# Performance work log

Hardware: AMD Instinct MI355X
Metric: run time of the kernel (lower is better)

Reference implementation:

```python
import jax, jax.numpy as jnp
import numpy as np

B, N, D, EMB, H, W = 32, 20, 512, 512, 64, 64
TEMP = 10.0
EPS_IN = 1e-5


def setup_inputs() -> dict:
    key = jax.random.key(0)
    ks = jax.random.split(key, 12)
    fvisu = jax.random.normal(ks[0], (B, D, H, W), dtype=jnp.float32)
    fword = jax.random.normal(ks[1], (B, N, D), dtype=jnp.float32)
    context_score = jax.random.uniform(ks[2], (B, N), dtype=jnp.float32)
    # contiguous valid-token mask: lengths in [3, N-1] so CLS/SEP zeroing stays in range
    lengths = jax.random.randint(ks[3], (B,), 3, N)  # < N
    word_mask = (jnp.arange(N)[None, :] < lengths[:, None]).astype(jnp.int32)
    # params (kaiming-ish scale)
    def kinit(k, shape, fan_in):
        return jax.random.normal(k, shape, dtype=jnp.float32) * np.sqrt(2.0 / fan_in)
    attn_map_w = kinit(ks[4], (EMB // 2, D), D)          # Conv1d(512,256,1)
    attn_map_b = jnp.zeros((EMB // 2,), jnp.float32)
    attn_score_w = kinit(ks[5], (EMB // 2,), EMB // 2)   # Conv1d(256,1,1)
    attn_score_b = jnp.zeros((), jnp.float32)
    gamma_w = kinit(ks[6], (2 * EMB, D), D)              # Linear(512, 1024)
    gamma_b = jnp.zeros((2 * EMB,), jnp.float32)
    conv1_w = kinit(ks[7], (EMB, D), D)                  # Conv2d(512,512,1)
    conv1_b = jnp.zeros((EMB,), jnp.float32)
    return {
        "fvisu": fvisu, "fword": fword, "context_score": context_score,
        "attn_map_w": attn_map_w, "attn_map_b": attn_map_b,
        "attn_score_w": attn_score_w, "attn_score_b": attn_score_b,
        "gamma_w": gamma_w, "gamma_b": gamma_b,
        "conv1_w": conv1_w, "conv1_b": conv1_b,
        "word_mask": word_mask,
    }


def mask_softmax(attn_score, word_mask):
    # score = softmax(attn_score * T) over words
    score = jax.nn.softmax(attn_score * TEMP, axis=1)
    n = attn_score.shape[1]
    idx = jnp.arange(n)[None, :]
    m = word_mask[:, :n].astype(jnp.float32)
    m = m * (idx != 0)                                   # zero CLS
    s = m.sum(axis=1).astype(jnp.int32)                  # sum AFTER zeroing pos 0
    m = m * (idx != s[:, None])                          # zero SEP (last valid)
    ms = score * m
    return ms / (ms.sum(axis=1, keepdims=True) + 1e-8)


def reference(fvisu, fword, context_score, attn_map_w, attn_map_b,
              attn_score_w, attn_score_b, gamma_w, gamma_b,
              conv1_w, conv1_b, word_mask):
    # fword: [B,N,D] -> fw: [B,D,N]
    fw = jnp.transpose(fword, (0, 2, 1))
    # tile_visu: mean over spatial -> [B,D,1]
    tile_visu = jnp.mean(fvisu.reshape(fvisu.shape[0], fvisu.shape[1], -1), axis=2, keepdims=True)
    # prod fusion
    context_tile = tile_visu * fw * context_score[:, None, :]           # [B,D,N]
    attn_feat = jnp.tanh(jnp.einsum('oc,bcn->bon', attn_map_w, context_tile) + attn_map_b[None, :, None])
    attn_score = jnp.einsum('c,bcn->bn', attn_score_w, attn_feat) + attn_score_b  # [B,N]
    mask_score = mask_softmax(attn_score, word_mask)
    attn_lang_my = mask_score[:, None, :] * fw                          # [B,D,N]
    attn_lang = jnp.einsum('bn,bnd->bd', mask_score, fword)             # [B,D]
    # FiLM params
    film = attn_lang @ gamma_w.T + gamma_b                              # [B,2*EMB]
    gammas = jnp.tanh(film[:, :EMB])[:, :, None, None]
    betas = jnp.tanh(film[:, EMB:])[:, :, None, None]
    # conv1 (1x1) + InstanceNorm2d (no affine)
    fmodu = jnp.einsum('oc,bchw->bohw', conv1_w, fvisu) + conv1_b[None, :, None, None]
    mu = jnp.mean(fmodu, axis=(2, 3), keepdims=True)
    var = jnp.var(fmodu, axis=(2, 3), keepdims=True)
    fmodu = (fmodu - mu) * jax.lax.rsqrt(var + EPS_IN)
    fmodu = jax.nn.relu(gammas * fmodu + betas)
    return fmodu, attn_lang_my, attn_score
```

## Files before the change

kernel.cpp:

```cpp
#include <hip/hip_runtime.h>
#include <hip/hip_bf16.h>
#include <stdint.h>

#define NW 20
#define CD 512

typedef __attribute__((ext_vector_type(8))) short bhalf8;
typedef __attribute__((ext_vector_type(4))) float floatx4;

__device__ __forceinline__ uint16_t f2bf(float f){
    __hip_bfloat16 h = __float2bfloat16(f);
    return __builtin_bit_cast(uint16_t, h);
}
__device__ __forceinline__ float bf2f(uint16_t u){
    return __uint_as_float(((uint32_t)u) << 16);
}
__device__ __forceinline__ int hsw(int r){ return ((r >> 1) ^ (r >> 2)) & 7; }

__device__ __forceinline__ void gload16(const void* g, void* l){
    __builtin_amdgcn_global_load_lds(
        (const __attribute__((address_space(1))) uint32_t*)g,
        (__attribute__((address_space(3))) uint32_t*)l, 16, 0, 0);
}

__global__ void GroundTextBlock_context_49761491091856_kernel(int* p){ if (p) *p = 0; }

__global__ __launch_bounds__(256) void kprep(const float* __restrict__ w,
                                             uint16_t* __restrict__ warr){
    int ot = blockIdx.x >> 3, ks = blockIdx.x & 7;
    uint16_t* dst = warr + (size_t)blockIdx.x * 8192;
    for (int i = threadIdx.x; i < 8192; i += 256){
        int o = i >> 6, ke = i & 63;
        float v = w[(size_t)(ot * 128 + o) * 512 + ks * 64 + ke];
        int byteoff = o * 128 + ((((ke >> 3) ^ hsw(o)) << 4)) + ((ke & 7) << 1);
        dst[byteoff >> 1] = f2bf(v);
    }
}

__global__ __launch_bounds__(256) void kprepB(const float* __restrict__ fvisu,
                                              float* __restrict__ out0){
    __shared__ __align__(16) uint8_t Bb[16384];
    __shared__ float tsum[CD];

    int b = blockIdx.x >> 5, jt = blockIdx.x & 31;
    int t = threadIdx.x, lane = t & 63;
    int cs0 = t >> 5, js = t & 31;
    int j0 = jt * 128;

    for (int ks = 0; ks < 8; ++ks){
        if (ks) __syncthreads();
        int k0 = ks * 64;
        #pragma unroll
        for (int blk = 0; blk < 2; ++blk){
            int cs = cs0 + blk * 8;
            float va[4][4];
            #pragma unroll
            for (int ci = 0; ci < 4; ++ci){
                const float* src = fvisu + (((size_t)(b * CD + k0 + cs * 4 + ci)) << 12) + j0 + js * 4;
                float4 v = *(const float4*)src;
                va[ci][0] = v.x; va[ci][1] = v.y; va[ci][2] = v.z; va[ci][3] = v.w;
            }
            #pragma unroll
            for (int ci = 0; ci < 4; ++ci){
                float s = va[ci][0] + va[ci][1] + va[ci][2] + va[ci][3];
                s += __shfl_xor(s, 1);  s += __shfl_xor(s, 2);
                s += __shfl_xor(s, 4);  s += __shfl_xor(s, 8);
                s += __shfl_xor(s, 16);
                if ((lane & 31) == 0) tsum[k0 + cs * 4 + ci] = s;
            }
            int unit = cs >> 1, half = cs & 1;
            #pragma unroll
            for (int jj = 0; jj < 4; ++jj){
                int j = js * 4 + jj;
                uint2 p;
                p.x = (uint32_t)f2bf(va[0][jj]) | ((uint32_t)f2bf(va[1][jj]) << 16);
                p.y = (uint32_t)f2bf(va[2][jj]) | ((uint32_t)f2bf(va[3][jj]) << 16);
                *(uint2*)(Bb + j * 128 + ((unit ^ hsw(j)) << 4) + half * 8) = p;
            }
        }
        __syncthreads();
        #pragma unroll
        for (int it = 0; it < 4; ++it){
            int off = it * 4096 + t * 16;
            int rrow = jt * 16 + ks * 2 + (off >> 13);
            uint8_t* dst = (uint8_t*)out0 + (((size_t)(b * CD + rrow)) << 14) + 8192 + (off & 8191);
            *(float4*)dst = *(const float4*)(Bb + off);
        }
    }
    __syncthreads();
    float* tp = out0 + (((size_t)(b * CD + jt)) << 12);
    tp[t] = tsum[t];
    tp[t + 256] = tsum[t + 256];
}

__global__ __launch_bounds__(256) void kgemm(const uint16_t* __restrict__ warr,
                                             float* __restrict__ out0){
    __shared__ __align__(16) uint8_t Ab[16384];
    __shared__ __align__(16) uint8_t Bb[16384];

    int lid = (int)((blockIdx.x & 7) * 512 + (blockIdx.x >> 3));
    int ot = lid & 3, jt = (lid >> 2) & 31, b = lid >> 7;

    int t = threadIdx.x;
    int lane = t & 63, wv = t >> 6;
    int wr = wv >> 1, wc = wv & 1;
    int l15 = lane & 15, l4 = lane >> 4;
    int j0 = jt * 128;

    floatx4 acc[4][4];
    #pragma unroll
    for (int m = 0; m < 4; ++m)
        #pragma unroll
        for (int n = 0; n < 4; ++n)
            acc[m][n] = (floatx4){0.f, 0.f, 0.f, 0.f};

    for (int ks = 0; ks < 8; ++ks){
        if (ks) __syncthreads();
        {
            const uint8_t* asrc = (const uint8_t*)warr + (size_t)(ot * 8 + ks) * 16384;
            #pragma unroll
            for (int it = 0; it < 4; ++it){
                int lin = it * 4096 + t * 16;
                gload16(asrc + lin, Ab + lin);
            }
        }
        #pragma unroll
        for (int it = 0; it < 4; ++it){
            int off = it * 4096 + t * 16;
            int rrow = jt * 16 + ks * 2 + (off >> 13);
            const uint8_t* src = (const uint8_t*)out0 + (((size_t)(b * CD + rrow)) << 14) + 8192 + (off & 8191);
            gload16(src, Bb + off);
        }
        __syncthreads();
        #pragma unroll
        for (int ksl = 0; ksl < 2; ++ksl){
            bhalf8 af[4], bfr[4];
            #pragma unroll
            for (int m = 0; m < 4; ++m){
                int o = wr * 64 + m * 16 + l15;
                int u = (ksl * 4 + l4) ^ hsw(o);
                af[m] = *(const bhalf8*)(Ab + o * 128 + (u << 4));
            }
            #pragma unroll
            for (int n = 0; n < 4; ++n){
                int j = wc * 64 + n * 16 + l15;
                int u = (ksl * 4 + l4) ^ hsw(j);
                bfr[n] = *(const bhalf8*)(Bb + j * 128 + (u << 4));
            }
            #pragma unroll
            for (int m = 0; m < 4; ++m)
                #pragma unroll
                for (int n = 0; n < 4; ++n)
                    acc[m][n] = __builtin_amdgcn_mfma_f32_16x16x32_bf16(af[m], bfr[n], acc[m][n], 0, 0, 0);
        }
    }
    uint16_t* sbase = (uint16_t*)out0;
    #pragma unroll
    for (int m = 0; m < 4; ++m){
        #pragma unroll
        for (int r = 0; r < 4; ++r){
            int o = ot * 128 + wr * 64 + m * 16 + l4 * 4 + r;
            uint16_t* row = sbase + ((size_t)(b * CD + o) << 13);
            #pragma unroll
            for (int n = 0; n < 4; ++n)
                row[j0 + wc * 64 + n * 16 + l15] = f2bf(acc[m][n][r]);
        }
    }
}

__global__ __launch_bounds__(256) void kattn(
    const float* __restrict__ fword, const float* __restrict__ cscore,
    const float* __restrict__ amw, const float* __restrict__ amb,
    const float* __restrict__ asw, const float* __restrict__ asb,
    const float* __restrict__ gw, const float* __restrict__ gb,
    const int* __restrict__ wmask, const float* __restrict__ out0,
    float* __restrict__ out1, float* __restrict__ out2,
    float* __restrict__ gam_arr, float* __restrict__ bet_arr)
{
    int b = blockIdx.x, t = threadIdx.x;
    __shared__ __align__(16) float fws[NW][CD];
    __shared__ __align__(16) float tl[CD];
    __shared__ __align__(16) float al[CD];
    __shared__ float css[NW];
    __shared__ int wm[NW];
    __shared__ float wred[4][NW];
    __shared__ float sc[NW];
    __shared__ float ms[NW];

    #pragma unroll
    for (int dd = 0; dd < 2; ++dd){
        int c = t + dd * 256;
        float s = 0.f;
        #pragma unroll 8
        for (int j2 = 0; j2 < 32; ++j2)
            s += out0[(((size_t)(b * CD + j2)) << 12) + c];
        tl[c] = s * (1.f / 4096.f);
    }
    {
        const float4* src = (const float4*)(fword + (size_t)b * NW * CD);
        float4* dst = (float4*)&fws[0][0];
        for (int i = t; i < NW * CD / 4; i += 256) dst[i] = src[i];
    }
    if (t < NW){ css[t] = cscore[b * NW + t]; wm[t] = wmask[b * NW + t]; }
    __syncthreads();

    int o = t;
    float a[NW];
    #pragma unroll
    for (int n = 0; n < NW; ++n) a[n] = 0.f;
    {
        const float4* wrp = (const float4*)(amw + (size_t)o * CD);
        for (int c4 = 0; c4 < 128; ++c4){
            float4 wvv = wrp[c4];
            float4 tv = *(const float4*)(tl + c4 * 4);
            float wtx = wvv.x * tv.x, wty = wvv.y * tv.y, wtz = wvv.z * tv.z, wtw = wvv.w * tv.w;
            #pragma unroll
            for (int n = 0; n < NW; ++n){
                const float4 f = *(const float4*)(&fws[n][c4 * 4]);
                a[n] += wtx * f.x + wty * f.y + wtz * f.z + wtw * f.w;
            }
        }
    }
    {
        float aswo = asw[o], ambo = amb[o];
        #pragma unroll
        for (int n = 0; n < NW; ++n){
            float fo = aswo * tanhf(a[n] * css[n] + ambo);
            #pragma unroll
            for (int m = 1; m <= 32; m <<= 1) fo += __shfl_xor(fo, m);
            if ((t & 63) == 0) wred[t >> 6][n] = fo;
        }
    }
    __syncthreads();
    if (t < NW){
        float s = asb[0] + wred[0][t] + wred[1][t] + wred[2][t] + wred[3][t];
        sc[t] = s;
        out2[b * NW + t] = s;
    }
    __syncthreads();
    if (t < 64){
        float logit = (t < NW) ? sc[t] * 10.f : -1e30f;
        float mx = logit;
        #pragma unroll
        for (int m = 32; m >= 1; m >>= 1) mx = fmaxf(mx, __shfl_xor(mx, m));
        float e = (t < NW) ? expf(logit - mx) : 0.f;
        float den = e;
        #pragma unroll
        for (int m = 32; m >= 1; m >>= 1) den += __shfl_xor(den, m);
        float p = e / den;
        float m0 = (t > 0 && t < NW) ? (float)wm[t] : 0.f;
        float cnt = m0;
        #pragma unroll
        for (int m = 32; m >= 1; m >>= 1) cnt += __shfl_xor(cnt, m);
        int sidx = (int)(cnt + 0.5f);
        float m1 = (t == sidx) ? 0.f : m0;
        float msv = p * m1;
        float d2 = msv;
        #pragma unroll
        for (int m = 32; m >= 1; m >>= 1) d2 += __shfl_xor(d2, m);
        d2 += 1e-8f;
        if (t < NW) ms[t] = msv / d2;
    }
    __syncthreads();
    #pragma unroll
    for (int dd = 0; dd < 2; ++dd){
        int d = t + dd * 256;
        float acc_ = 0.f;
        float pk[NW];
        #pragma unroll
        for (int n = 0; n < NW; ++n){
            float v = ms[n] * fws[n][d];
            acc_ += v;
            pk[n] = v;
        }
        al[d] = acc_;
        float4* dst = (float4*)(out1 + (size_t)b * CD * NW + (size_t)d * NW);
        #pragma unroll
        for (int i = 0; i < NW / 4; ++i)
            dst[i] = make_float4(pk[i * 4], pk[i * 4 + 1], pk[i * 4 + 2], pk[i * 4 + 3]);
    }
    __syncthreads();
    #pragma unroll
    for (int kk = 0; kk < 4; ++kk){
        int k = kk * 256 + t;
        const float4* gr = (const float4*)(gw + (size_t)k * CD);
        float s = gb[k];
        for (int c4 = 0; c4 < 128; ++c4){
            float4 g4 = gr[c4];
            float4 a4 = *(const float4*)(al + c4 * 4);
            s += g4.x * a4.x + g4.y * a4.y + g4.z * a4.z + g4.w * a4.w;
        }
        float tv = tanhf(s);
        if (k < CD) gam_arr[b * CD + k] = tv;
        else        bet_arr[b * CD + (k - CD)] = tv;
    }
}

__global__ __launch_bounds__(256) void knormstat(
    float* __restrict__ out0, const float* __restrict__ gam_arr,
    const float* __restrict__ bet_arr)
{
    int bo = blockIdx.x, t = threadIdx.x;
    const uint16_t* srow = (const uint16_t*)out0 + ((size_t)bo << 13);
    float x[16];
    float s = 0.f, q = 0.f;
    #pragma unroll
    for (int h = 0; h < 2; ++h){
        uint4 v = *(const uint4*)(srow + (size_t)(h * 256 + t) * 8);
        uint32_t w[4] = {v.x, v.y, v.z, v.w};
        #pragma unroll
        for (int i = 0; i < 4; ++i){
            float x0 = bf2f((uint16_t)(w[i] & 0xffffu));
            float x1 = bf2f((uint16_t)(w[i] >> 16));
            x[h * 8 + i * 2]     = x0;
            x[h * 8 + i * 2 + 1] = x1;
            s += x0 + x1; q += x0 * x0 + x1 * x1;
        }
    }
    #pragma unroll
    for (int m = 1; m <= 32; m <<= 1){ s += __shfl_xor(s, m); q += __shfl_xor(q, m); }
    __shared__ float ss[4], qq[4];
    if ((t & 63) == 0){ ss[t >> 6] = s; qq[t >> 6] = q; }
    __syncthreads();
    float S = ss[0] + ss[1] + ss[2] + ss[3];
    float Q = qq[0] + qq[1] + qq[2] + qq[3];
    float mu = S * (1.f / 4096.f);
    float var = Q * (1.f / 4096.f) - mu * mu;
    float rs = rsqrtf(var + 1e-5f);
    float g = gam_arr[bo], be = bet_arr[bo];
    float4* drow = (float4*)(out0 + ((size_t)bo << 12));
    #pragma unroll
    for (int h = 0; h < 2; ++h){
        #pragma unroll
        for (int gix = 0; gix < 2; ++gix){
            float4 w4;
            w4.x = fmaxf(0.f, g * ((x[h * 8 + gix * 4 + 0] - mu) * rs) + be);
            w4.y = fmaxf(0.f, g * ((x[h * 8 + gix * 4 + 1] - mu) * rs) + be);
            w4.z = fmaxf(0.f, g * ((x[h * 8 + gix * 4 + 2] - mu) * rs) + be);
            w4.w = fmaxf(0.f, g * ((x[h * 8 + gix * 4 + 3] - mu) * rs) + be);
            drow[(size_t)(h * 256 + t) * 2 + gix] = w4;
        }
    }
}

extern "C" void kernel_launch(void* const* d_in, const int* in_sizes, int n_in,
                              void* d_out, int out_size, void* d_ws, size_t ws_size,
                              hipStream_t stream)
{
    const float* fvisu  = (const float*)d_in[0];
    const float* fword  = (const float*)d_in[1];
    const float* cscore = (const float*)d_in[2];
    const float* amw    = (const float*)d_in[3];
    const float* amb    = (const float*)d_in[4];
    const float* asw    = (const float*)d_in[5];
    const float* asb    = (const float*)d_in[6];
    const float* gw     = (const float*)d_in[7];
    const float* gb     = (const float*)d_in[8];
    const float* cw     = (const float*)d_in[9];
    const int* wmask    = (const int*)d_in[11];

    float* out0 = (float*)d_out;
    float* out1 = out0 + (size_t)67108864;
    float* out2 = out1 + (size_t)327680;

    uint8_t* ws = (uint8_t*)d_ws;
    uint16_t* warr = (uint16_t*)ws;
    float* gam_arr = (float*)(ws + 524288);
    float* bet_arr = (float*)(ws + 589824);

    kprep<<<32, 256, 0, stream>>>(cw, warr);
    kprepB<<<1024, 256, 0, stream>>>(fvisu, out0);
    kattn<<<32, 256, 0, stream>>>(fword, cscore, amw, amb, asw, asb, gw, gb, wmask,
                                  out0, out1, out2, gam_arr, bet_arr);
    kgemm<<<4096, 256, 0, stream>>>(warr, out0);
    knormstat<<<16384, 256, 0, stream>>>(out0, gam_arr, bet_arr);
}
```

Baseline: 386.1 us.

## Fuse fvisu bf16 conversion and mean reduction into the conv1 GEMM kernel

The separate prep kernel that turned fvisu into a bf16 staging copy inside the output buffer is removed. The GEMM kernel now reads fp32 fvisu directly, converts it to bf16 in LDS, and its ot==0 blocks compute the per-channel spatial partial sums. Those sums go to the unused second half of the output rows, and the attention kernel now runs after the GEMM and reads them from there. This removes the write and re-read of the bf16 staging tensor and one kernel launch. In exchange, each fvisu tile is loaded and converted by four blocks (one per output tile), and the B operand load becomes synchronous register loads instead of async LDS loads.

```diff
diff --git a/kernel.cpp b/kernel.cpp
--- a/kernel.cpp
+++ b/kernel.cpp
@@ -37,18 +37,40 @@
     }
 }
 
-__global__ __launch_bounds__(256) void kprepB(const float* __restrict__ fvisu,
-                                              float* __restrict__ out0){
+__global__ __launch_bounds__(256) void kgemm(const float* __restrict__ fvisu,
+                                             const uint16_t* __restrict__ warr,
+                                             float* __restrict__ out0){
+    __shared__ __align__(16) uint8_t Ab[16384];
     __shared__ __align__(16) uint8_t Bb[16384];
     __shared__ float tsum[CD];
 
-    int b = blockIdx.x >> 5, jt = blockIdx.x & 31;
-    int t = threadIdx.x, lane = t & 63;
+    int lid = (int)((blockIdx.x & 7) * 512 + (blockIdx.x >> 3));
+    int ot = lid & 3, jt = (lid >> 2) & 31, b = lid >> 7;
+
+    int t = threadIdx.x;
+    int lane = t & 63, wv = t >> 6;
+    int wr = wv >> 1, wc = wv & 1;
+    int l15 = lane & 15, l4 = lane >> 4;
     int cs0 = t >> 5, js = t & 31;
     int j0 = jt * 128;
 
+    floatx4 acc[4][4];
+    #pragma unroll
+    for (int m = 0; m < 4; ++m)
+        #pragma unroll
+        for (int n = 0; n < 4; ++n)
+            acc[m][n] = (floatx4){0.f, 0.f, 0.f, 0.f};
+
     for (int ks = 0; ks < 8; ++ks){
         if (ks) __syncthreads();
+        {
+            const uint8_t* asrc = (const uint8_t*)warr + (size_t)(ot * 8 + ks) * 16384;
+            #pragma unroll
+            for (int it = 0; it < 4; ++it){
+                int lin = it * 4096 + t * 16;
+                gload16(asrc + lin, Ab + lin);
+            }
+        }
         int k0 = ks * 64;
         #pragma unroll
         for (int blk = 0; blk < 2; ++blk){
@@ -60,13 +82,15 @@
                 float4 v = *(const float4*)src;
                 va[ci][0] = v.x; va[ci][1] = v.y; va[ci][2] = v.z; va[ci][3] = v.w;
             }
-            #pragma unroll
-            for (int ci = 0; ci < 4; ++ci){
-                float s = va[ci][0] + va[ci][1] + va[ci][2] + va[ci][3];
-                s += __shfl_xor(s, 1);  s += __shfl_xor(s, 2);
-                s += __shfl_xor(s, 4);  s += __shfl_xor(s, 8);
-                s += __shfl_xor(s, 16);
-                if ((lane & 31) == 0) tsum[k0 + cs * 4 + ci] = s;
+            if (ot == 0){
+                #pragma unroll
+                for (int ci = 0; ci < 4; ++ci){
+                    float s = va[ci][0] + va[ci][1] + va[ci][2] + va[ci][3];
+                    s += __shfl_xor(s, 1);  s += __shfl_xor(s, 2);
+                    s += __shfl_xor(s, 4);  s += __shfl_xor(s, 8);
+                    s += __shfl_xor(s, 16);
+                    if ((lane & 31) == 0) tsum[k0 + cs * 4 + ci] = s;
+                }
             }
             int unit = cs >> 1, half = cs & 1;
             #pragma unroll
@@ -80,59 +104,6 @@
         }
         __syncthreads();
         #pragma unroll
-        for (int it = 0; it < 4; ++it){
-            int off = it * 4096 + t * 16;
-            int rrow = jt * 16 + ks * 2 + (off >> 13);
-            uint8_t* dst = (uint8_t*)out0 + (((size_t)(b * CD + rrow)) << 14) + 8192 + (off & 8191);
-            *(float4*)dst = *(const float4*)(Bb + off);
-        }
-    }
-    __syncthreads();
-    float* tp = out0 + (((size_t)(b * CD + jt)) << 12);
-    tp[t] = tsum[t];
-    tp[t + 256] = tsum[t + 256];
-}
-
-__global__ __launch_bounds__(256) void kgemm(const uint16_t* __restrict__ warr,
-                                             float* __restrict__ out0){
-    __shared__ __align__(16) uint8_t Ab[16384];
-    __shared__ __align__(16) uint8_t Bb[16384];
-
-    int lid = (int)((blockIdx.x & 7) * 512 + (blockIdx.x >> 3));
-    int ot = lid & 3, jt = (lid >> 2) & 31, b = lid >> 7;
-
-    int t = threadIdx.x;
-    int lane = t & 63, wv = t >> 6;
-    int wr = wv >> 1, wc = wv & 1;
-    int l15 = lane & 15, l4 = lane >> 4;
-    int j0 = jt * 128;
-
-    floatx4 acc[4][4];
-    #pragma unroll
-    for (int m = 0; m < 4; ++m)
-        #pragma unroll
-        for (int n = 0; n < 4; ++n)
-            acc[m][n] = (floatx4){0.f, 0.f, 0.f, 0.f};
-
-    for (int ks = 0; ks < 8; ++ks){
-        if (ks) __syncthreads();
-        {
-            const uint8_t* asrc = (const uint8_t*)warr + (size_t)(ot * 8 + ks) * 16384;
-            #pragma unroll
-            for (int it = 0; it < 4; ++it){
-                int lin = it * 4096 + t * 16;
-                gload16(asrc + lin, Ab + lin);
-            }
-        }
-        #pragma unroll
-        for (int it = 0; it < 4; ++it){
-            int off = it * 4096 + t * 16;
-            int rrow = jt * 16 + ks * 2 + (off >> 13);
-            const uint8_t* src = (const uint8_t*)out0 + (((size_t)(b * CD + rrow)) << 14) + 8192 + (off & 8191);
-            gload16(src, Bb + off);
-        }
-        __syncthreads();
-        #pragma unroll
         for (int ksl = 0; ksl < 2; ++ksl){
             bhalf8 af[4], bfr[4];
             #pragma unroll
@@ -153,6 +124,12 @@
                 for (int n = 0; n < 4; ++n)
                     acc[m][n] = __builtin_amdgcn_mfma_f32_16x16x32_bf16(af[m], bfr[n], acc[m][n], 0, 0, 0);
         }
+    }
+    if (ot == 0){
+        __syncthreads();
+        float* tp = out0 + (((size_t)(b * CD + jt)) << 12) + 2048;
+        tp[t] = tsum[t];
+        tp[t + 256] = tsum[t + 256];
     }
     uint16_t* sbase = (uint16_t*)out0;
     #pragma unroll
@@ -193,7 +170,7 @@
         float s = 0.f;
         #pragma unroll 8
         for (int j2 = 0; j2 < 32; ++j2)
-            s += out0[(((size_t)(b * CD + j2)) << 12) + c];
+            s += out0[(((size_t)(b * CD + j2)) << 12) + 2048 + c];
         tl[c] = s * (1.f / 4096.f);
     }
     {
@@ -369,9 +346,8 @@
     float* bet_arr = (float*)(ws + 589824);
 
     kprep<<<32, 256, 0, stream>>>(cw, warr);
-    kprepB<<<1024, 256, 0, stream>>>(fvisu, out0);
+    kgemm<<<4096, 256, 0, stream>>>(fvisu, warr, out0);
     kattn<<<32, 256, 0, stream>>>(fword, cscore, amw, amb, asw, asb, gw, gb, wmask,
                                   out0, out1, out2, gam_arr, bet_arr);
-    kgemm<<<4096, 256, 0, stream>>>(warr, out0);
     knormstat<<<16384, 256, 0, stream>>>(out0, gam_arr, bet_arr);
 }
```

Result: faster. 360.6 us (median of 3 runs) (-6.6%).
